# Kernel tuning notes

Hardware: AMD Instinct MI355X
Metric: run time of the kernel (lower is better)

## Reference

```python
import jax, jax.numpy as jnp
import numpy as np

BINS = 10  # constructor default


def setup_inputs() -> dict:
    key = jax.random.key(0)
    k1, k2 = jax.random.split(key)
    bs, cla = 262144, 128
    # probabilities strictly inside (0,1) so log terms are finite
    u = jax.random.uniform(k1, (bs, cla), dtype=jnp.float32)
    inputs = 0.01 + 0.98 * u
    # binary 0/1 targets as floats
    targets = jnp.round(jax.random.uniform(k2, (bs, cla), dtype=jnp.float32))
    return {"inputs": inputs, "targets": targets}


def reference(inputs, targets):
    bins = BINS
    tot = jnp.asarray(inputs.size, jnp.float32)  # bs * cla

    # gradient-norm proxy g = |p.detach() - t|, in [0, 1]
    g = jnp.abs(jax.lax.stop_gradient(inputs) - targets)

    # edges are i/bins with the last edge nudged to 1+1e-6, so
    # floor(g*bins) clipped to bins-1 reproduces the per-bin masks exactly
    idx = jnp.clip(jnp.floor(g * bins).astype(jnp.int32), 0, bins - 1)

    # histogram counts per bin (fused scatter-add instead of the Python loop)
    counts = jnp.zeros((bins,), jnp.float32).at[idx.ravel()].add(1.0)

    n = jnp.sum(counts > 0).astype(jnp.float32)  # number of non-empty bins
    w_per_bin = jnp.where(counts > 0, tot / jnp.maximum(counts, 1.0), 0.0)
    weights = w_per_bin[idx] / jnp.maximum(n, 1.0)
    weights = jax.lax.stop_gradient(weights)  # weights built from detached g

    # elementwise binary cross entropy on probabilities
    bce = -(targets * jnp.log(inputs) + (1.0 - targets) * jnp.log1p(-inputs))
    loss = jnp.sum(weights * bce) / tot
    return loss
```

## Files before the change

### kernel.cpp

```cpp
#include <hip/hip_runtime.h>

#define BINS 10


__device__ __forceinline__ void elem(float p, float t,
                                     float* __restrict__ sb,
                                     unsigned int* __restrict__ cw)
{
    float g  = fabsf(p - t);
    float l2 = __log2f(1.0f - g);
    int   bi = (int)(g * 10.0f);
#pragma unroll
    for (int b = 0; b < BINS; ++b) {
        bool hit = (bi == b);
        unsigned long long m = __ballot(hit);
        sb[b] += hit ? l2 : 0.0f;
        cw[b] += (unsigned int)__popcll(m);
    }
}

__device__ __forceinline__ void proc4v(const float4 p, const float4 t,
                                       float* __restrict__ sb,
                                       unsigned int* __restrict__ cw)
{
    elem(p.x, t.x, sb, cw); elem(p.y, t.y, sb, cw);
    elem(p.z, t.z, sb, cw); elem(p.w, t.w, sb, cw);
}

__global__ __launch_bounds__(256, 8) void ghm_partial(
    const float4* __restrict__ p4,
    const float4* __restrict__ t4,
    float* __restrict__ gsum,
    unsigned int* __restrict__ gcnt,
    int n4)
{
    float        sb[BINS];
    unsigned int cw[BINS];
#pragma unroll
    for (int b = 0; b < BINS; ++b) { sb[b] = 0.0f; cw[b] = 0u; }

    const int tid    = threadIdx.x;
    const int start  = blockIdx.x * blockDim.x + tid;
    const int stride = gridDim.x * blockDim.x;
    const int ngrp   = n4 / (4 * stride);

    int i = start;
    for (int grp = 0; grp < ngrp; ++grp, i += 4 * stride) {
        float4 P0 = p4[i];
        float4 T0 = t4[i];
        float4 P1 = p4[i + stride];
        float4 T1 = t4[i + stride];
        float4 P2 = p4[i + 2 * stride];
        float4 T2 = t4[i + 2 * stride];
        float4 P3 = p4[i + 3 * stride];
        float4 T3 = t4[i + 3 * stride];
        __builtin_amdgcn_sched_barrier(0);
        proc4v(P0, T0, sb, cw);
        proc4v(P1, T1, sb, cw);
        proc4v(P2, T2, sb, cw);
        proc4v(P3, T3, sb, cw);
    }
    for (int j = start + ngrp * 4 * stride; j < n4; j += stride) {
        float4 p = p4[j], t = t4[j];
        proc4v(p, t, sb, cw);
    }

    __shared__ float        redS[BINS];
    __shared__ unsigned int redC[BINS];
    if (tid < BINS) { redS[tid] = 0.0f; redC[tid] = 0u; }
    __syncthreads();

    const int lane = tid & 63;
#pragma unroll
    for (int b = 0; b < BINS; ++b) {
        float s = sb[b];
#pragma unroll
        for (int off = 32; off > 0; off >>= 1) s += __shfl_down(s, off);
        if (lane == 0) {
            atomicAdd(&redS[b], s);
            atomicAdd(&redC[b], cw[b]);
        }
    }
    __syncthreads();
    if (tid < BINS) {
        atomicAdd(&gsum[tid], redS[tid]);
        atomicAdd(&gcnt[tid], redC[tid]);
    }
}

__global__ void ghm_finalize(const float* __restrict__ gsum,
                             const unsigned int* __restrict__ gcnt,
                             float* __restrict__ out)
{
    if (threadIdx.x == 0 && blockIdx.x == 0) {
        int n = 0;
#pragma unroll
        for (int b = 0; b < BINS; ++b) n += (gcnt[b] > 0u) ? 1 : 0;
        float nn = (float)(n > 0 ? n : 1);
        float acc = 0.0f;
#pragma unroll
        for (int b = 0; b < BINS; ++b) {
            if (gcnt[b] > 0u)
                acc += gsum[b] / ((float)gcnt[b] * nn);
        }
        out[0] = -0.6931471805599453f * acc;
    }
}

extern "C" void kernel_launch(void* const* d_in, const int* in_sizes, int n_in,
                              void* d_out, int out_size, void* d_ws, size_t ws_size,
                              hipStream_t stream)
{
    const float* p = (const float*)d_in[0];
    const float* t = (const float*)d_in[1];
    const int n  = in_sizes[0];
    const int n4 = n >> 2;

    float*        gsum = (float*)d_ws;
    unsigned int* gcnt = (unsigned int*)((char*)d_ws + BINS * sizeof(float));

    hipMemsetAsync(d_ws, 0, BINS * (sizeof(float) + sizeof(unsigned int)), stream);

    const int threads = 256;
    const int blocks  = 2048;
    ghm_partial<<<blocks, threads, 0, stream>>>(
        (const float4*)p, (const float4*)t, gsum, gcnt, n4);

    ghm_finalize<<<1, 64, 0, stream>>>(gsum, gcnt, (float*)d_out);
}
```

Baseline: 290.2 us.

## Replace per-bin ballot loop with LDS column histogram and packed counters

```diff
diff --git a/kernel.cpp b/kernel.cpp
--- a/kernel.cpp
+++ b/kernel.cpp
@@ -4,27 +4,22 @@
 
 
 __device__ __forceinline__ void elem(float p, float t,
-                                     float* __restrict__ sb,
-                                     unsigned int* __restrict__ cw)
+                                     float* __restrict__ col,
+                                     unsigned long long* __restrict__ pk)
 {
     float g  = fabsf(p - t);
     float l2 = __log2f(1.0f - g);
     int   bi = (int)(g * 10.0f);
-#pragma unroll
-    for (int b = 0; b < BINS; ++b) {
-        bool hit = (bi == b);
-        unsigned long long m = __ballot(hit);
-        sb[b] += hit ? l2 : 0.0f;
-        cw[b] += (unsigned int)__popcll(m);
-    }
+    *pk += 1ull << (6 * bi);
+    col[bi << 8] += l2;
 }
 
 __device__ __forceinline__ void proc4v(const float4 p, const float4 t,
-                                       float* __restrict__ sb,
-                                       unsigned int* __restrict__ cw)
+                                       float* __restrict__ col,
+                                       unsigned long long* __restrict__ pk)
 {
-    elem(p.x, t.x, sb, cw); elem(p.y, t.y, sb, cw);
-    elem(p.z, t.z, sb, cw); elem(p.w, t.w, sb, cw);
+    elem(p.x, t.x, col, pk); elem(p.y, t.y, col, pk);
+    elem(p.z, t.z, col, pk); elem(p.w, t.w, col, pk);
 }
 
 __global__ __launch_bounds__(256, 8) void ghm_partial(
@@ -34,12 +29,19 @@
     unsigned int* __restrict__ gcnt,
     int n4)
 {
-    float        sb[BINS];
+    __shared__ float hsum[BINS * 256];
+
+    const int tid = threadIdx.x;
+    for (int k = tid; k < BINS * 256; k += 256) hsum[k] = 0.0f;
+    __syncthreads();
+
+    unsigned long long pk = 0ull;
     unsigned int cw[BINS];
 #pragma unroll
-    for (int b = 0; b < BINS; ++b) { sb[b] = 0.0f; cw[b] = 0u; }
+    for (int b = 0; b < BINS; ++b) cw[b] = 0u;
 
-    const int tid    = threadIdx.x;
+    float* col = &hsum[tid];
+
     const int start  = blockIdx.x * blockDim.x + tid;
     const int stride = gridDim.x * blockDim.x;
     const int ngrp   = n4 / (4 * stride);
@@ -55,15 +57,32 @@
         float4 P3 = p4[i + 3 * stride];
         float4 T3 = t4[i + 3 * stride];
         __builtin_amdgcn_sched_barrier(0);
-        proc4v(P0, T0, sb, cw);
-        proc4v(P1, T1, sb, cw);
-        proc4v(P2, T2, sb, cw);
-        proc4v(P3, T3, sb, cw);
+        proc4v(P0, T0, col, &pk);
+        proc4v(P1, T1, col, &pk);
+        proc4v(P2, T2, col, &pk);
+        proc4v(P3, T3, col, &pk);
+        if (grp & 1) {
+#pragma unroll
+            for (int b = 0; b < BINS; ++b)
+                cw[b] += (unsigned int)((pk >> (6 * b)) & 63ull);
+            pk = 0ull;
+        }
     }
+#pragma unroll
+    for (int b = 0; b < BINS; ++b)
+        cw[b] += (unsigned int)((pk >> (6 * b)) & 63ull);
+    pk = 0ull;
+
     for (int j = start + ngrp * 4 * stride; j < n4; j += stride) {
         float4 p = p4[j], t = t4[j];
-        proc4v(p, t, sb, cw);
+        proc4v(p, t, col, &pk);
+#pragma unroll
+        for (int b = 0; b < BINS; ++b)
+            cw[b] += (unsigned int)((pk >> (6 * b)) & 63ull);
+        pk = 0ull;
     }
+
+    __syncthreads();
 
     __shared__ float        redS[BINS];
     __shared__ unsigned int redC[BINS];
@@ -73,12 +92,16 @@
     const int lane = tid & 63;
 #pragma unroll
     for (int b = 0; b < BINS; ++b) {
-        float s = sb[b];
+        float        s = hsum[(b << 8) + tid];
+        unsigned int c = cw[b];
 #pragma unroll
-        for (int off = 32; off > 0; off >>= 1) s += __shfl_down(s, off);
+        for (int off = 32; off > 0; off >>= 1) {
+            s += __shfl_down(s, off);
+            c += __shfl_down(c, off);
+        }
         if (lane == 0) {
             atomicAdd(&redS[b], s);
-            atomicAdd(&redC[b], cw[b]);
+            atomicAdd(&redC[b], c);
         }
     }
     __syncthreads();
```

Result: slower. 301.0 us (+3.7%).

## Replace per-bin wave ballots with packed per-thread counters and double-buffered loads

Applied to the files above, without the earlier changes.

```diff
diff --git a/kernel.cpp b/kernel.cpp
--- a/kernel.cpp
+++ b/kernel.cpp
@@ -5,29 +5,35 @@
 
 __device__ __forceinline__ void elem(float p, float t,
                                      float* __restrict__ sb,
-                                     unsigned int* __restrict__ cw)
+                                     unsigned long long* __restrict__ pk)
 {
     float g  = fabsf(p - t);
     float l2 = __log2f(1.0f - g);
     int   bi = (int)(g * 10.0f);
+    *pk += 1ull << (6 * bi);
 #pragma unroll
-    for (int b = 0; b < BINS; ++b) {
-        bool hit = (bi == b);
-        unsigned long long m = __ballot(hit);
-        sb[b] += hit ? l2 : 0.0f;
-        cw[b] += (unsigned int)__popcll(m);
-    }
+    for (int b = 0; b < BINS; ++b)
+        sb[b] += (bi == b) ? l2 : 0.0f;
 }
 
 __device__ __forceinline__ void proc4v(const float4 p, const float4 t,
                                        float* __restrict__ sb,
-                                       unsigned int* __restrict__ cw)
+                                       unsigned long long* __restrict__ pk)
 {
-    elem(p.x, t.x, sb, cw); elem(p.y, t.y, sb, cw);
-    elem(p.z, t.z, sb, cw); elem(p.w, t.w, sb, cw);
+    elem(p.x, t.x, sb, pk); elem(p.y, t.y, sb, pk);
+    elem(p.z, t.z, sb, pk); elem(p.w, t.w, sb, pk);
 }
 
-__global__ __launch_bounds__(256, 8) void ghm_partial(
+__device__ __forceinline__ void flushpk(unsigned long long* __restrict__ pk,
+                                        unsigned int* __restrict__ cw)
+{
+#pragma unroll
+    for (int b = 0; b < BINS; ++b)
+        cw[b] += (unsigned int)((*pk >> (6 * b)) & 63ull);
+    *pk = 0ull;
+}
+
+__global__ __launch_bounds__(256, 6) void ghm_partial(
     const float4* __restrict__ p4,
     const float4* __restrict__ t4,
     float* __restrict__ gsum,
@@ -36,33 +42,50 @@
 {
     float        sb[BINS];
     unsigned int cw[BINS];
+    unsigned long long pk = 0ull;
 #pragma unroll
     for (int b = 0; b < BINS; ++b) { sb[b] = 0.0f; cw[b] = 0u; }
 
     const int tid    = threadIdx.x;
     const int start  = blockIdx.x * blockDim.x + tid;
     const int stride = gridDim.x * blockDim.x;
-    const int ngrp   = n4 / (4 * stride);
+    const int nch    = n4 / (2 * stride);
 
     int i = start;
-    for (int grp = 0; grp < ngrp; ++grp, i += 4 * stride) {
-        float4 P0 = p4[i];
-        float4 T0 = t4[i];
-        float4 P1 = p4[i + stride];
-        float4 T1 = t4[i + stride];
-        float4 P2 = p4[i + 2 * stride];
-        float4 T2 = t4[i + 2 * stride];
-        float4 P3 = p4[i + 3 * stride];
-        float4 T3 = t4[i + 3 * stride];
-        __builtin_amdgcn_sched_barrier(0);
-        proc4v(P0, T0, sb, cw);
-        proc4v(P1, T1, sb, cw);
-        proc4v(P2, T2, sb, cw);
-        proc4v(P3, T3, sb, cw);
+    float4 PA0, TA0, PA1, TA1;
+    float4 PB0, TB0, PB1, TB1;
+
+    if (nch > 0) {
+        PA0 = p4[i];          TA0 = t4[i];
+        PA1 = p4[i + stride]; TA1 = t4[i + stride];
+        i += 2 * stride;
+        for (int c = 0; c + 2 <= nch; c += 2) {
+            PB0 = p4[i];          TB0 = t4[i];
+            PB1 = p4[i + stride]; TB1 = t4[i + stride];
+            i += 2 * stride;
+            __builtin_amdgcn_sched_barrier(0);
+            proc4v(PA0, TA0, sb, &pk);
+            proc4v(PA1, TA1, sb, &pk);
+            if (c + 2 < nch) {
+                PA0 = p4[i];          TA0 = t4[i];
+                PA1 = p4[i + stride]; TA1 = t4[i + stride];
+                i += 2 * stride;
+            }
+            __builtin_amdgcn_sched_barrier(0);
+            proc4v(PB0, TB0, sb, &pk);
+            proc4v(PB1, TB1, sb, &pk);
+            if (c & 2) flushpk(&pk, cw);
+        }
+        if (nch & 1) {
+            proc4v(PA0, TA0, sb, &pk);
+            proc4v(PA1, TA1, sb, &pk);
+        }
+        flushpk(&pk, cw);
     }
-    for (int j = start + ngrp * 4 * stride; j < n4; j += stride) {
+    for (int j = start + nch * 2 * stride; j < n4; j += stride) {
         float4 p = p4[j], t = t4[j];
-        proc4v(p, t, sb, cw);
+        proc4v(p, t, sb, &pk);
+        flushpk(&pk, cw);
     }
 
     __shared__ float        redS[BINS];
@@ -73,12 +96,16 @@
     const int lane = tid & 63;
 #pragma unroll
     for (int b = 0; b < BINS; ++b) {
-        float s = sb[b];
+        float        s = sb[b];
+        unsigned int c = cw[b];
 #pragma unroll
-        for (int off = 32; off > 0; off >>= 1) s += __shfl_down(s, off);
+        for (int off = 32; off > 0; off >>= 1) {
+            s += __shfl_down(s, off);
+            c += __shfl_down(c, off);
+        }
         if (lane == 0) {
             atomicAdd(&redS[b], s);
-            atomicAdd(&redC[b], cw[b]);
+            atomicAdd(&redC[b], c);
         }
     }
     __syncthreads();
```

New measurement: 325.2 us. 1.12x slower.
